# Kernel optimization log

Measured on AMD Instinct MI355X. Metric: run time of the kernel, lower is better.

The kernel has to match this reference:

```python
import jax, jax.numpy as jnp
import numpy as np

B, T, D = 4, 2048, 1024

def layer_norm(x, gamma, bias):
    # NOTE: faithfully reproduces the source's (buggy) LN: x - mu/sqrt(var), unbiased var
    mu = jnp.mean(x, axis=-1, keepdims=True)
    var = jnp.var(x, axis=-1, ddof=1, keepdims=True)
    return (x - mu / jnp.sqrt(var)) * gamma + bias

def setup_inputs() -> dict:
    key = jax.random.key(0)
    ks = jax.random.split(key, 8)
    scale = 1.0 / np.sqrt(D)
    return {
        'x': jax.random.normal(ks[0], (B, T, D), dtype=jnp.float32),
        'gamma1': jnp.ones((D,), jnp.float32),
        'beta1': jnp.zeros((D,), jnp.float32),
        'w_q': jax.random.uniform(ks[1], (D, D), jnp.float32, -scale, scale),
        'w_k': jax.random.uniform(ks[2], (D, D), jnp.float32, -scale, scale),
        'w_v': jax.random.uniform(ks[3], (D, D), jnp.float32, -scale, scale),
        'gamma2': jnp.ones((D,), jnp.float32),
        'beta2': jnp.zeros((D,), jnp.float32),
        'W1': jax.random.uniform(ks[4], (D, D), jnp.float32, -scale, scale),
        'b1': jnp.zeros((D,), jnp.float32),
        'W2': jax.random.uniform(ks[5], (D, D), jnp.float32, -scale, scale),
        'b2': jnp.zeros((D,), jnp.float32),
    }

def reference(x, gamma1, beta1, w_q, w_k, w_v, gamma2, beta2, W1, b1, W2, b2):
    d_model = x.shape[-1]
    t = x.shape[1]
    h = layer_norm(x, gamma1, beta1)
    q = jnp.einsum('btk,kd->btd', h, w_q)
    k = jnp.einsum('btk,kd->btd', h, w_k)
    v = jnp.einsum('btk,kd->btd', h, w_v)
    scale = 1.0 / jnp.sqrt(jnp.asarray(d_model, x.dtype))
    causal = jnp.tril(jnp.ones((t, t), dtype=bool))
    mask = jnp.where(causal, 0.0, -jnp.inf).astype(x.dtype)
    scores = jnp.einsum('bqd,bkd->bqk', q, k) * scale + mask
    attn = jax.nn.softmax(scores, axis=-1)
    y = jnp.einsum('bqt,btd->bqd', attn, v) + x
    h2 = layer_norm(y, gamma2, beta2)
    out = jnp.maximum(h2 @ W1 + b1, 0.0) @ W2 + b2
    return out + y
```

## Files before the change

kernel.cpp:

```cpp
#include <hip/hip_runtime.h>
#include <hip/hip_bf16.h>
#include <math.h>

using bf16 = __hip_bfloat16;

static constexpr int Bn = 4;
static constexpr int Tn = 2048;
static constexpr int Dn = 1024;

typedef __attribute__((ext_vector_type(8))) short bf16x8;
typedef __attribute__((ext_vector_type(4))) float f32x4;

__device__ __forceinline__ float ldf(float v) { return v; }
__device__ __forceinline__ float ldf(bf16 v) { return __bfloat162float(v); }
__device__ __forceinline__ bf16 f2b(float v) { return __float2bfloat16(v); }
__device__ __forceinline__ float b2f(short s) {
    return __uint_as_float(((unsigned)(unsigned short)s) << 16);
}
__device__ __forceinline__ short f2bs(float v) {
    bf16 t = __float2bfloat16(v);
    return *reinterpret_cast<short*>(&t);
}

template <typename T> __device__ __forceinline__ T from_float(float v);
template <> __device__ __forceinline__ float from_float<float>(float v) { return v; }
template <> __device__ __forceinline__ bf16 from_float<bf16>(float v) { return f2b(v); }

__device__ __forceinline__ void load4(const float* p, float* v) {
    const float4 t = *(const float4*)p;
    v[0] = t.x; v[1] = t.y; v[2] = t.z; v[3] = t.w;
}
__device__ __forceinline__ void load4(const bf16* p, float* v) {
    const short4 t = *(const short4*)p;
    v[0] = b2f(t.x); v[1] = b2f(t.y); v[2] = b2f(t.z); v[3] = b2f(t.w);
}

__device__ __forceinline__ void async_copy16(const bf16* g, bf16* l) {
    __builtin_amdgcn_global_load_lds(
        (const __attribute__((address_space(1))) void*)g,
        (__attribute__((address_space(3))) void*)l,
        16, 0, 0);
}

template <int BM, int BN, int MINW, typename OutT, typename ResT, bool RELU>
__global__ __launch_bounds__(256, MINW) void gemm_nt(
    const bf16* __restrict__ A, const bf16* __restrict__ Bm,
    OutT* __restrict__ C, const float* __restrict__ bias,
    const ResT* __restrict__ res,
    int M, int N, int K, int lda, int ldb, int ldc,
    long sA, long sB, long sC, long sR, int mode)
{
    const int bm = blockIdx.y, bn = blockIdx.x, bz = blockIdx.z;
    if (mode == 1 && bn * BN > bm * BM + (BM - 1)) return;
    const int kend = bm * BM + BM;
    const int kmax = (mode == 2) ? (kend < K ? kend : K) : K;

    const bf16* Ab = A + (size_t)bz * sA;
    const bf16* Bb = Bm + (size_t)bz * sB;

    constexpr int WROWS = BM / 64;
    constexpr int WCOLS = 4 / WROWS;
    constexpr int TM = 64;
    constexpr int TN = BN / WCOLS;
    constexpr int MT = TM / 16;
    constexpr int NT = TN / 16;
    constexpr int nA = BM / 16;
    constexpr int nB = BN / 16;

    __shared__ __align__(16) bf16 As[2 * BM * 32];
    __shared__ __align__(16) bf16 Bs[2 * BN * 32];

    const int tid = threadIdx.x;
    const int wave = tid >> 6;
    const int lane = tid & 63;
    const int wm = wave / WCOLS;
    const int wn = wave % WCOLS;

    f32x4 acc[MT][NT] = {};

    const int lr = lane >> 2;
    const int lc = (lane & 3) * 8;
    const bf16* gAc[nA / 4]; bf16* lAc[nA / 4];
    const bf16* gBc[nB / 4]; bf16* lBc[nB / 4];
#pragma unroll
    for (int i = 0; i < nA / 4; ++i) {
        const int c = wave + 4 * i;
        gAc[i] = Ab + (size_t)(bm * BM + c * 16 + lr) * lda + lc;
        lAc[i] = &As[c * 512];
    }
#pragma unroll
    for (int i = 0; i < nB / 4; ++i) {
        const int c = wave + 4 * i;
        gBc[i] = Bb + (size_t)(bn * BN + c * 16 + lr) * ldb + lc;
        lBc[i] = &Bs[c * 512];
    }

    const int arow = lane & 15;
    const int kq = (lane >> 4) * 8;

    for (int k0 = 0; k0 < kmax; k0 += 64) {
#pragma unroll
        for (int hh = 0; hh < 2; ++hh) {
#pragma unroll
            for (int i = 0; i < nA / 4; ++i)
                async_copy16(gAc[i] + k0 + 32 * hh, lAc[i] + hh * (BM * 32));
#pragma unroll
            for (int i = 0; i < nB / 4; ++i)
                async_copy16(gBc[i] + k0 + 32 * hh, lBc[i] + hh * (BN * 32));
        }
        __syncthreads();

#pragma unroll
        for (int hh = 0; hh < 2; ++hh) {
            const bf16* Ah = As + hh * (BM * 32);
            const bf16* Bh = Bs + hh * (BN * 32);
            bf16x8 af[MT], bfm[NT];
#pragma unroll
            for (int t = 0; t < MT; ++t)
                af[t] = *(const bf16x8*)&Ah[(wm * TM + t * 16 + arow) * 32 + kq];
#pragma unroll
            for (int t = 0; t < NT; ++t)
                bfm[t] = *(const bf16x8*)&Bh[(wn * TN + t * 16 + arow) * 32 + kq];
#pragma unroll
            for (int mt = 0; mt < MT; ++mt)
#pragma unroll
                for (int nt = 0; nt < NT; ++nt)
                    acc[mt][nt] = __builtin_amdgcn_mfma_f32_16x16x32_bf16(
                        af[mt], bfm[nt], acc[mt][nt], 0, 0, 0);
        }
        __syncthreads();
    }

    OutT* Cb = C + (size_t)bz * sC;
    const ResT* Rb = res ? (res + (size_t)bz * sR) : nullptr;
    const int rowBase = bm * BM + wm * TM;
    const int colBase = bn * BN + wn * TN;
    const int qrow = (lane >> 4) * 4;
    const int ccol = lane & 15;

#pragma unroll
    for (int mt = 0; mt < MT; ++mt) {
#pragma unroll
        for (int nt = 0; nt < NT; ++nt) {
            const int cc = colBase + nt * 16 + ccol;
            const float bv = bias ? bias[cc] : 0.0f;
#pragma unroll
            for (int r = 0; r < 4; ++r) {
                const int rr = rowBase + mt * 16 + qrow + r;
                float v = acc[mt][nt][r] + bv;
                if (RELU) v = fmaxf(v, 0.0f);
                if (Rb) v += ldf(Rb[(size_t)rr * ldc + cc]);
                Cb[(size_t)rr * ldc + cc] = from_float<OutT>(v);
            }
        }
    }
}

template <typename InT>
__global__ __launch_bounds__(256) void ln_kernel(
    const InT* __restrict__ x, const float* __restrict__ gamma,
    const float* __restrict__ beta, bf16* __restrict__ out)
{
    const int row = blockIdx.x;
    const int tid = threadIdx.x;
    const int j = tid * 4;
    const InT* xr = x + (size_t)row * Dn;

    float v[4];
    load4(xr + j, v);
    float s = v[0] + v[1] + v[2] + v[3];
    float sq = v[0] * v[0] + v[1] * v[1] + v[2] * v[2] + v[3] * v[3];
#pragma unroll
    for (int o = 32; o > 0; o >>= 1) {
        s += __shfl_down(s, o);
        sq += __shfl_down(sq, o);
    }
    __shared__ float red[2][4];
    const int lane = tid & 63, w = tid >> 6;
    if (lane == 0) { red[0][w] = s; red[1][w] = sq; }
    __syncthreads();
    s  = red[0][0] + red[0][1] + red[0][2] + red[0][3];
    sq = red[1][0] + red[1][1] + red[1][2] + red[1][3];
    const float mean = s / (float)Dn;
    const float var = (sq - s * s / (float)Dn) / (float)(Dn - 1);
    const float coef = mean * rsqrtf(var);

    const float4 g = *(const float4*)(gamma + j);
    const float4 be = *(const float4*)(beta + j);
    short4 o;
    o.x = f2bs((v[0] - coef) * g.x + be.x);
    o.y = f2bs((v[1] - coef) * g.y + be.y);
    o.z = f2bs((v[2] - coef) * g.z + be.z);
    o.w = f2bs((v[3] - coef) * g.w + be.w);
    *(short4*)(out + (size_t)row * Dn + j) = o;
}

__global__ __launch_bounds__(256) void softmax_kernel(
    const bf16* __restrict__ S, bf16* __restrict__ P)
{
    const int r = blockIdx.x;
    const int b = r >> 11, i = r & (Tn - 1);
    const bf16* srow = S + ((size_t)b * Tn + i) * Tn;
    bf16* prow = P + ((size_t)b * Tn + i) * Tn;
    const int L = i + 1;
    const float scale = 0.03125f;
    const int tid = threadIdx.x;
    const int j0 = tid * 8;
    const int lane = tid & 63, w = tid >> 6;

    const bf16x8 sv = *(const bf16x8*)(srow + j0);
    float v[8];
#pragma unroll
    for (int e = 0; e < 8; ++e)
        v[e] = (j0 + e < L) ? b2f(sv[e]) * scale : -INFINITY;

    float mx = v[0];
#pragma unroll
    for (int e = 1; e < 8; ++e) mx = fmaxf(mx, v[e]);
#pragma unroll
    for (int o = 32; o > 0; o >>= 1) mx = fmaxf(mx, __shfl_down(mx, o));
    __shared__ float rmx[4], rsum[4];
    if (lane == 0) rmx[w] = mx;
    __syncthreads();
    mx = fmaxf(fmaxf(rmx[0], rmx[1]), fmaxf(rmx[2], rmx[3]));

    float p[8], sum = 0.f;
#pragma unroll
    for (int e = 0; e < 8; ++e) { p[e] = __expf(v[e] - mx); sum += p[e]; }
#pragma unroll
    for (int o = 32; o > 0; o >>= 1) sum += __shfl_down(sum, o);
    if (lane == 0) rsum[w] = sum;
    __syncthreads();
    sum = rsum[0] + rsum[1] + rsum[2] + rsum[3];
    const float inv = 1.0f / sum;

    bf16x8 pv;
#pragma unroll
    for (int e = 0; e < 8; ++e) pv[e] = f2bs(p[e] * inv);
    *(bf16x8*)(prow + j0) = pv;
}

template <typename InT>
__global__ __launch_bounds__(256) void transpose_kernel(
    const InT* __restrict__ in, bf16* __restrict__ out,
    int ldi, int ldo, long inStride, long outStride)
{
    __shared__ bf16 tile[32][33];
    const int z = blockIdx.z;
    const InT* src = in + (size_t)z * inStride;
    bf16* dst = out + (size_t)z * outStride;
    const int c0 = blockIdx.x * 32, r0 = blockIdx.y * 32;
    const int tx = threadIdx.x & 31;
    const int ty = threadIdx.x >> 5;
#pragma unroll
    for (int dy = 0; dy < 32; dy += 8)
        tile[ty + dy][tx] = f2b(ldf(src[(size_t)(r0 + ty + dy) * ldi + (c0 + tx)]));
    __syncthreads();
#pragma unroll
    for (int dy = 0; dy < 32; dy += 8)
        dst[(size_t)(c0 + ty + dy) * ldo + (r0 + tx)] = tile[tx][ty + dy];
}

extern "C" void kernel_launch(void* const* d_in, const int* in_sizes, int n_in,
                              void* d_out, int out_size, void* d_ws, size_t ws_size,
                              hipStream_t stream) {
    const float* x      = (const float*)d_in[0];
    const float* gamma1 = (const float*)d_in[1];
    const float* beta1  = (const float*)d_in[2];
    const float* w_q    = (const float*)d_in[3];
    const float* w_k    = (const float*)d_in[4];
    const float* w_v    = (const float*)d_in[5];
    const float* gamma2 = (const float*)d_in[6];
    const float* beta2  = (const float*)d_in[7];
    const float* W1     = (const float*)d_in[8];
    const float* b1     = (const float*)d_in[9];
    const float* W2     = (const float*)d_in[10];
    const float* b2     = (const float*)d_in[11];
    float* out = (float*)d_out;

    char* ws = (char*)d_ws;
    size_t off = 0;
    auto alloc = [&](size_t bytes) {
        char* p = ws + off;
        off += (bytes + 255) & ~(size_t)255;
        return p;
    };
    const size_t BT = (size_t)Bn * Tn;
    bf16* h     = (bf16*)alloc(BT * Dn * 2);
    bf16* qkv   = (bf16*)alloc(BT * 3 * Dn * 2);
    bf16* vt    = (bf16*)alloc(BT * Dn * 2);
    bf16* wqkvt = (bf16*)alloc((size_t)3 * Dn * Dn * 2);
    bf16* wt1   = (bf16*)alloc((size_t)Dn * Dn * 2);
    bf16* wt2   = (bf16*)alloc((size_t)Dn * Dn * 2);
    bf16* S     = (bf16*)alloc((size_t)Bn * Tn * Tn * 2);
    bf16* P     = (bf16*)alloc((size_t)Bn * Tn * Tn * 2);
    bf16* y     = S;
    bf16* h2    = h;
    bf16* mid   = qkv;

    const dim3 blk(256);
    const long TD   = (long)Tn * Dn;
    const long TT   = (long)Tn * Tn;
    const long TD3  = (long)Tn * 3 * Dn;

    transpose_kernel<float><<<dim3(32, 32, 1), blk, 0, stream>>>(w_q, wqkvt,                Dn, Dn, 0, 0);
    transpose_kernel<float><<<dim3(32, 32, 1), blk, 0, stream>>>(w_k, wqkvt + 1024 * 1024,  Dn, Dn, 0, 0);
    transpose_kernel<float><<<dim3(32, 32, 1), blk, 0, stream>>>(w_v, wqkvt + 2048 * 1024,  Dn, Dn, 0, 0);
    transpose_kernel<float><<<dim3(32, 32, 1), blk, 0, stream>>>(W1, wt1, Dn, Dn, 0, 0);
    transpose_kernel<float><<<dim3(32, 32, 1), blk, 0, stream>>>(W2, wt2, Dn, Dn, 0, 0);

    ln_kernel<float><<<dim3((unsigned)BT), blk, 0, stream>>>(x, gamma1, beta1, h);

    gemm_nt<128, 128, 3, bf16, float, false><<<dim3(24, 64, 1), blk, 0, stream>>>(
        h, wqkvt, qkv, nullptr, nullptr,
        (int)BT, 3 * Dn, Dn, Dn, Dn, 3 * Dn, 0, 0, 0, 0, 0);

    transpose_kernel<bf16><<<dim3(32, 64, Bn), blk, 0, stream>>>(
        qkv + 2048, vt, 3 * Dn, Tn, TD3, TD);

    gemm_nt<128, 128, 3, bf16, float, false><<<dim3(16, 16, Bn), blk, 0, stream>>>(
        qkv, qkv + 1024, S, nullptr, nullptr,
        Tn, Tn, Dn, 3 * Dn, 3 * Dn, Tn, TD3, TD3, TT, 0, 1);

    softmax_kernel<<<dim3((unsigned)BT), blk, 0, stream>>>(S, P);

    gemm_nt<64, 128, 4, bf16, float, false><<<dim3(8, 32, Bn), blk, 0, stream>>>(
        P, vt, y, nullptr, x,
        Tn, Dn, Tn, Tn, Tn, Dn, TT, TD, TD, TD, 2);

    ln_kernel<bf16><<<dim3((unsigned)BT), blk, 0, stream>>>(y, gamma2, beta2, h2);

    gemm_nt<128, 128, 3, bf16, float, true><<<dim3(8, 64, 1), blk, 0, stream>>>(
        h2, wt1, mid, b1, nullptr,
        (int)BT, Dn, Dn, Dn, Dn, Dn, 0, 0, 0, 0, 0);

    gemm_nt<128, 128, 3, float, bf16, false><<<dim3(8, 64, 1), blk, 0, stream>>>(
        mid, wt2, out, b2, y,
        (int)BT, Dn, Dn, Dn, Dn, Dn, 0, 0, 0, 0, 0);
}
```

Baseline: 387.8 us.

## Fuse V transpose into QKV GEMM epilogue and batch weight transposes

The QKV GEMM epilogue now writes the V columns straight into a transposed V buffer, which removes the separate V transpose kernel and shrinks the QK buffer to two column blocks. The five weight transposes become one launch over a z-grid, and softmax skips loading score chunks that lie entirely past the causal boundary. The PV GEMM moves to 128-row tiles, and every GEMM's launch-bounds occupancy hint goes from 3 to 4 waves. The transposed V stores are strided short4 writes, which may be less coalesced than the old transpose kernel's writes.

```diff
diff --git a/kernel.cpp b/kernel.cpp
--- a/kernel.cpp
+++ b/kernel.cpp
@@ -42,11 +42,11 @@
         16, 0, 0);
 }
 
-template <int BM, int BN, int MINW, typename OutT, typename ResT, bool RELU>
+template <int BM, int BN, int MINW, typename OutT, typename ResT, bool RELU, bool VSPLIT>
 __global__ __launch_bounds__(256, MINW) void gemm_nt(
     const bf16* __restrict__ A, const bf16* __restrict__ Bm,
     OutT* __restrict__ C, const float* __restrict__ bias,
-    const ResT* __restrict__ res,
+    const ResT* __restrict__ res, bf16* __restrict__ vtp,
     int M, int N, int K, int lda, int ldb, int ldc,
     long sA, long sB, long sC, long sR, int mode)
 {
@@ -131,13 +131,33 @@
         __syncthreads();
     }
 
-    OutT* Cb = C + (size_t)bz * sC;
-    const ResT* Rb = res ? (res + (size_t)bz * sR) : nullptr;
     const int rowBase = bm * BM + wm * TM;
     const int colBase = bn * BN + wn * TN;
     const int qrow = (lane >> 4) * 4;
     const int ccol = lane & 15;
 
+    if (VSPLIT && bn * BN >= 2048) {
+#pragma unroll
+        for (int mt = 0; mt < MT; ++mt) {
+            const int t0 = rowBase + mt * 16 + qrow;
+            const int b = t0 >> 11, t = t0 & (Tn - 1);
+            bf16* vb = vtp + (size_t)b * Dn * Tn + t;
+#pragma unroll
+            for (int nt = 0; nt < NT; ++nt) {
+                const int d = colBase + nt * 16 + ccol - 2048;
+                short4 o;
+                o.x = f2bs(acc[mt][nt][0]);
+                o.y = f2bs(acc[mt][nt][1]);
+                o.z = f2bs(acc[mt][nt][2]);
+                o.w = f2bs(acc[mt][nt][3]);
+                *(short4*)(vb + (size_t)d * Tn) = o;
+            }
+        }
+        return;
+    }
+
+    OutT* Cb = C + (size_t)bz * sC;
+    const ResT* Rb = res ? (res + (size_t)bz * sR) : nullptr;
 #pragma unroll
     for (int mt = 0; mt < MT; ++mt) {
 #pragma unroll
@@ -208,11 +228,16 @@
     const int j0 = tid * 8;
     const int lane = tid & 63, w = tid >> 6;
 
-    const bf16x8 sv = *(const bf16x8*)(srow + j0);
     float v[8];
-#pragma unroll
-    for (int e = 0; e < 8; ++e)
-        v[e] = (j0 + e < L) ? b2f(sv[e]) * scale : -INFINITY;
+    if (j0 < L) {
+        const bf16x8 sv = *(const bf16x8*)(srow + j0);
+#pragma unroll
+        for (int e = 0; e < 8; ++e)
+            v[e] = (j0 + e < L) ? b2f(sv[e]) * scale : -INFINITY;
+    } else {
+#pragma unroll
+        for (int e = 0; e < 8; ++e) v[e] = -INFINITY;
+    }
 
     float mx = v[0];
 #pragma unroll
@@ -240,25 +265,24 @@
     *(bf16x8*)(prow + j0) = pv;
 }
 
-template <typename InT>
-__global__ __launch_bounds__(256) void transpose_kernel(
-    const InT* __restrict__ in, bf16* __restrict__ out,
-    int ldi, int ldo, long inStride, long outStride)
+struct WPtrs { const float* p[5]; };
+
+__global__ __launch_bounds__(256) void wtrans_kernel(WPtrs wp, bf16* __restrict__ dst)
 {
     __shared__ bf16 tile[32][33];
     const int z = blockIdx.z;
-    const InT* src = in + (size_t)z * inStride;
-    bf16* dst = out + (size_t)z * outStride;
+    const float* src = wp.p[z];
+    bf16* d = dst + (size_t)z * Dn * Dn;
     const int c0 = blockIdx.x * 32, r0 = blockIdx.y * 32;
     const int tx = threadIdx.x & 31;
     const int ty = threadIdx.x >> 5;
 #pragma unroll
     for (int dy = 0; dy < 32; dy += 8)
-        tile[ty + dy][tx] = f2b(ldf(src[(size_t)(r0 + ty + dy) * ldi + (c0 + tx)]));
+        tile[ty + dy][tx] = f2b(src[(size_t)(r0 + ty + dy) * Dn + (c0 + tx)]);
     __syncthreads();
 #pragma unroll
     for (int dy = 0; dy < 32; dy += 8)
-        dst[(size_t)(c0 + ty + dy) * ldo + (r0 + tx)] = tile[tx][ty + dy];
+        d[(size_t)(c0 + ty + dy) * Dn + (r0 + tx)] = tile[tx][ty + dy];
 }
 
 extern "C" void kernel_launch(void* const* d_in, const int* in_sizes, int n_in,
@@ -286,55 +310,47 @@
         return p;
     };
     const size_t BT = (size_t)Bn * Tn;
-    bf16* h     = (bf16*)alloc(BT * Dn * 2);
-    bf16* qkv   = (bf16*)alloc(BT * 3 * Dn * 2);
-    bf16* vt    = (bf16*)alloc(BT * Dn * 2);
-    bf16* wqkvt = (bf16*)alloc((size_t)3 * Dn * Dn * 2);
-    bf16* wt1   = (bf16*)alloc((size_t)Dn * Dn * 2);
-    bf16* wt2   = (bf16*)alloc((size_t)Dn * Dn * 2);
-    bf16* S     = (bf16*)alloc((size_t)Bn * Tn * Tn * 2);
-    bf16* P     = (bf16*)alloc((size_t)Bn * Tn * Tn * 2);
-    bf16* y     = S;
-    bf16* h2    = h;
-    bf16* mid   = qkv;
+    bf16* h    = (bf16*)alloc(BT * Dn * 2);
+    bf16* qk   = (bf16*)alloc(BT * 2 * Dn * 2);
+    bf16* vt   = (bf16*)alloc(BT * Dn * 2);
+    bf16* wbuf = (bf16*)alloc((size_t)5 * Dn * Dn * 2);
+    bf16* S    = (bf16*)alloc((size_t)Bn * Tn * Tn * 2);
+    bf16* P    = (bf16*)alloc((size_t)Bn * Tn * Tn * 2);
+    bf16* y    = S;
+    bf16* h2   = h;
+    bf16* mid  = qk;
 
     const dim3 blk(256);
-    const long TD   = (long)Tn * Dn;
-    const long TT   = (long)Tn * Tn;
-    const long TD3  = (long)Tn * 3 * Dn;
-
-    transpose_kernel<float><<<dim3(32, 32, 1), blk, 0, stream>>>(w_q, wqkvt,                Dn, Dn, 0, 0);
-    transpose_kernel<float><<<dim3(32, 32, 1), blk, 0, stream>>>(w_k, wqkvt + 1024 * 1024,  Dn, Dn, 0, 0);
-    transpose_kernel<float><<<dim3(32, 32, 1), blk, 0, stream>>>(w_v, wqkvt + 2048 * 1024,  Dn, Dn, 0, 0);
-    transpose_kernel<float><<<dim3(32, 32, 1), blk, 0, stream>>>(W1, wt1, Dn, Dn, 0, 0);
-    transpose_kernel<float><<<dim3(32, 32, 1), blk, 0, stream>>>(W2, wt2, Dn, Dn, 0, 0);
+    const long TD  = (long)Tn * Dn;
+    const long TT  = (long)Tn * Tn;
+    const long TD2 = (long)Tn * 2 * Dn;
+
+    WPtrs wp; wp.p[0] = w_q; wp.p[1] = w_k; wp.p[2] = w_v; wp.p[3] = W1; wp.p[4] = W2;
+    wtrans_kernel<<<dim3(32, 32, 5), blk, 0, stream>>>(wp, wbuf);
 
     ln_kernel<float><<<dim3((unsigned)BT), blk, 0, stream>>>(x, gamma1, beta1, h);
 
-    gemm_nt<128, 128, 3, bf16, float, false><<<dim3(24, 64, 1), blk, 0, stream>>>(
-        h, wqkvt, qkv, nullptr, nullptr,
-        (int)BT, 3 * Dn, Dn, Dn, Dn, 3 * Dn, 0, 0, 0, 0, 0);
-
-    transpose_kernel<bf16><<<dim3(32, 64, Bn), blk, 0, stream>>>(
-        qkv + 2048, vt, 3 * Dn, Tn, TD3, TD);
-
-    gemm_nt<128, 128, 3, bf16, float, false><<<dim3(16, 16, Bn), blk, 0, stream>>>(
-        qkv, qkv + 1024, S, nullptr, nullptr,
-        Tn, Tn, Dn, 3 * Dn, 3 * Dn, Tn, TD3, TD3, TT, 0, 1);
+    gemm_nt<128, 128, 4, bf16, float, false, true><<<dim3(24, 64, 1), blk, 0, stream>>>(
+        h, wbuf, qk, nullptr, nullptr, vt,
+        (int)BT, 3 * Dn, Dn, Dn, Dn, 2 * Dn, 0, 0, 0, 0, 0);
+
+    gemm_nt<128, 128, 4, bf16, float, false, false><<<dim3(16, 16, Bn), blk, 0, stream>>>(
+        qk, qk + 1024, S, nullptr, nullptr, nullptr,
+        Tn, Tn, Dn, 2 * Dn, 2 * Dn, Tn, TD2, TD2, TT, 0, 1);
 
     softmax_kernel<<<dim3((unsigned)BT), blk, 0, stream>>>(S, P);
 
-    gemm_nt<64, 128, 4, bf16, float, false><<<dim3(8, 32, Bn), blk, 0, stream>>>(
-        P, vt, y, nullptr, x,
+    gemm_nt<128, 128, 4, bf16, float, false, false><<<dim3(8, 16, Bn), blk, 0, stream>>>(
+        P, vt, y, nullptr, x, nullptr,
         Tn, Dn, Tn, Tn, Tn, Dn, TT, TD, TD, TD, 2);
 
     ln_kernel<bf16><<<dim3((unsigned)BT), blk, 0, stream>>>(y, gamma2, beta2, h2);
 
-    gemm_nt<128, 128, 3, bf16, float, true><<<dim3(8, 64, 1), blk, 0, stream>>>(
-        h2, wt1, mid, b1, nullptr,
+    gemm_nt<128, 128, 4, bf16, float, true, false><<<dim3(8, 64, 1), blk, 0, stream>>>(
+        h2, wbuf + (size_t)3 * Dn * Dn, mid, b1, nullptr, nullptr,
         (int)BT, Dn, Dn, Dn, Dn, Dn, 0, 0, 0, 0, 0);
 
-    gemm_nt<128, 128, 3, float, bf16, false><<<dim3(8, 64, 1), blk, 0, stream>>>(
-        mid, wt2, out, b2, y,
+    gemm_nt<128, 128, 4, float, bf16, false, false><<<dim3(8, 64, 1), blk, 0, stream>>>(
+        mid, wbuf + (size_t)4 * Dn * Dn, out, b2, y, nullptr,
         (int)BT, Dn, Dn, Dn, Dn, Dn, 0, 0, 0, 0, 0);
 }
```

New measurement: 363.6 us. -6.3%, faster.
